# Optimization experiments

Measured on AMD Instinct MI355X. Metric: run time of the kernel, lower is better.

## Reference

```python
import jax, jax.numpy as jnp
import numpy as np

NH, NKV, HD = 16, 4, 64   # n_heads, n_kv_heads, head_dim
N_REP = NH // NKV
EPS = 1e-6


def rms_norm(x, w):
    var = jnp.mean(x.astype(jnp.float32) ** 2, axis=-1, keepdims=True)
    return (x.astype(jnp.float32) * jax.lax.rsqrt(var + EPS)).astype(x.dtype) * w


def rotate_half(x):
    x1, x2 = jnp.split(x, 2, axis=-1)
    return jnp.concatenate([-x2, x1], axis=-1)


def setup_inputs() -> dict:
    key = jax.random.key(0)
    ks = jax.random.split(key, 6)
    B, S, H = 2, 2048, 2048
    x = jax.random.normal(ks[0], (B, S, H), dtype=jnp.float32)
    # RoPE tables [S, HD]
    inv_freq = 1.0 / (10000.0 ** (jnp.arange(0, HD, 2, dtype=jnp.float32) / HD))
    freqs = jnp.arange(S, dtype=jnp.float32)[:, None] * inv_freq[None, :]
    emb = jnp.concatenate([freqs, freqs], axis=-1)
    cos, sin = jnp.cos(emb), jnp.sin(emb)
    scale = 0.02
    wq = jax.random.normal(ks[1], (H, NH * HD), dtype=jnp.float32) * scale
    wk = jax.random.normal(ks[2], (H, NKV * HD), dtype=jnp.float32) * scale
    wv = jax.random.normal(ks[3], (H, NKV * HD), dtype=jnp.float32) * scale
    wo = jax.random.normal(ks[4], (NH * HD, H), dtype=jnp.float32) * scale
    q_norm_w = jnp.ones((HD,), dtype=jnp.float32)
    k_norm_w = jnp.ones((HD,), dtype=jnp.float32)
    return {"x": x, "cos": cos, "sin": sin, "wq": wq, "wk": wk, "wv": wv,
            "wo": wo, "q_norm_w": q_norm_w, "k_norm_w": k_norm_w}


def reference(x, cos, sin, wq, wk, wv, wo, q_norm_w, k_norm_w):
    B, S, H = x.shape
    # QKV projections + per-head RMSNorm on q/k
    q = rms_norm((x @ wq).reshape(B, S, NH, HD), q_norm_w)
    k = rms_norm((x @ wk).reshape(B, S, NKV, HD), k_norm_w)
    v = (x @ wv).reshape(B, S, NKV, HD)
    # RoPE (broadcast over heads)
    c = cos[None, :S, None, :]
    s = sin[None, :S, None, :]
    q = q * c + rotate_half(q) * s
    k = k * c + rotate_half(k) * s
    # prefill with S == window_size: no KV eviction, T == S -> causal mask
    k = jnp.repeat(k, N_REP, axis=2)  # [B,S,NH,HD]
    v = jnp.repeat(v, N_REP, axis=2)
    scores = jnp.einsum('bqhd,bkhd->bhqk', q, k) / jnp.sqrt(jnp.float32(HD))
    causal = jnp.triu(jnp.full((S, S), -jnp.inf, dtype=scores.dtype), 1)
    scores = scores + causal
    attn = jax.nn.softmax(scores.astype(jnp.float32), axis=-1).astype(q.dtype)
    out = jnp.einsum('bhqk,bkhd->bqhd', attn, v).reshape(B, S, NH * HD)
    return out @ wo
```

## Files before the change

kernel.cpp:

```cpp
#include <hip/hip_runtime.h>

typedef float floatx4 __attribute__((ext_vector_type(4)));
typedef __bf16 bfx8 __attribute__((ext_vector_type(8)));
typedef __bf16 bfx4 __attribute__((ext_vector_type(4)));

constexpr int B_ = 2, S_ = 2048, H_ = 2048, NH_ = 16, NKV_ = 4, HD_ = 64;
constexpr int M_ = B_ * S_;
constexpr int NQKV_ = NH_ * HD_ + 2 * NKV_ * HD_;
constexpr int HQ_ = NH_ * HD_;
constexpr int XP_ = 2112;
constexpr int AP_ = 1088;
constexpr int VP_ = 2112;
constexpr int QKV_ELEMS_ = M_ * NQKV_;

#define GLB(p) ((const __attribute__((address_space(1))) void*)(p))
#define LDS(p) ((__attribute__((address_space(3))) void*)(p))

__global__ __launch_bounds__(256) void prep_kernel(const float* __restrict__ x,
                                                   const float* __restrict__ wq,
                                                   const float* __restrict__ wk,
                                                   const float* __restrict__ wv,
                                                   const float* __restrict__ wo,
                                                   __bf16* __restrict__ xbf,
                                                   __bf16* __restrict__ wqkvT,
                                                   __bf16* __restrict__ woT) {
  __shared__ float tile[32][33];
  int bid = blockIdx.x;
  if (bid < M_) {
    const float4* s = (const float4*)(x + (size_t)bid * H_);
    __bf16* d = xbf + (size_t)bid * XP_;
#pragma unroll
    for (int i = 0; i < 2; i++) {
      int c = i * 256 + threadIdx.x;
      float4 v = s[c];
      bfx4 o;
      o[0] = (__bf16)v.x; o[1] = (__bf16)v.y; o[2] = (__bf16)v.z; o[3] = (__bf16)v.w;
      *(bfx4*)(d + c * 4) = o;
    }
    return;
  }
  bid -= M_;
  const float* src; __bf16* dst; int N, dstOff, pitch, nbx;
  if (bid < 2048)      { src = wq; dst = wqkvT; N = 1024; dstOff = 0;    pitch = XP_; nbx = 32; }
  else if (bid < 2560) { bid -= 2048; src = wk; dst = wqkvT; N = 256; dstOff = 1024; pitch = XP_; nbx = 8; }
  else if (bid < 3072) { bid -= 2560; src = wv; dst = wqkvT; N = 256; dstOff = 1280; pitch = XP_; nbx = 8; }
  else                 { bid -= 3072; src = wo; dst = woT;   N = 2048; dstOff = 0;   pitch = AP_; nbx = 64; }
  int n0 = (bid % nbx) * 32, k0 = (bid / nbx) * 32;
  int tx = threadIdx.x & 31, ty = threadIdx.x >> 5;
#pragma unroll
  for (int r = 0; r < 32; r += 8)
    tile[ty + r][tx] = src[(size_t)(k0 + ty + r) * N + n0 + tx];
  __syncthreads();
#pragma unroll
  for (int r = 0; r < 32; r += 8)
    dst[(size_t)(n0 + ty + r + dstOff) * pitch + k0 + tx] = (__bf16)tile[tx][ty + r];
}

__global__ __launch_bounds__(512) void gemm_bf16_f32(const __bf16* __restrict__ A,
                                                     const __bf16* __restrict__ Bt,
                                                     float* __restrict__ C,
                                                     int M, int N, int K,
                                                     int lda, int ldb, int ldc,
                                                     unsigned long long cstride) {
  __shared__ __align__(16) __bf16 As[256 * 64];
  __shared__ __align__(16) __bf16 Bs[128 * 64];
  int wid = threadIdx.x >> 6, lane = threadIdx.x & 63;
  int l15 = lane & 15, quad = lane >> 4;
  int wm = (wid >> 1) * 64, wn = (wid & 1) * 64;
  int m0 = blockIdx.y * 256, n0 = blockIdx.x * 128;
  int kb0 = blockIdx.z * K;
  C += (size_t)blockIdx.z * cstride;
  int srow_off = lane >> 3;
  int gphys = lane & 7;
  floatx4 acc[4][4] = {};
  for (int kb = kb0; kb < kb0 + K; kb += 64) {
#pragma unroll
    for (int j = 0; j < 4; j++) {
      int rbase = j * 64 + wid * 8;
      int row = rbase + srow_off;
      int glog = gphys ^ (row & 7);
      const __bf16* ga = &A[(size_t)(m0 + row) * lda + kb + glog * 8];
      __builtin_amdgcn_global_load_lds(GLB(ga), LDS(&As[rbase * 64]), 16, 0, 0);
    }
#pragma unroll
    for (int j = 0; j < 2; j++) {
      int rbase = j * 64 + wid * 8;
      int row = rbase + srow_off;
      int glog = gphys ^ (row & 7);
      const __bf16* gb = &Bt[(size_t)(n0 + row) * ldb + kb + glog * 8];
      __builtin_amdgcn_global_load_lds(GLB(gb), LDS(&Bs[rbase * 64]), 16, 0, 0);
    }
    __syncthreads();
#pragma unroll
    for (int kk = 0; kk < 64; kk += 32) {
      int cgq = (kk >> 3) + quad;
      bfx8 af[4], bfr[4];
#pragma unroll
      for (int mi = 0; mi < 4; mi++) {
        int row = wm + mi * 16 + l15;
        af[mi] = *(const bfx8*)&As[row * 64 + (cgq ^ (row & 7)) * 8];
      }
#pragma unroll
      for (int ni = 0; ni < 4; ni++) {
        int row = wn + ni * 16 + l15;
        bfr[ni] = *(const bfx8*)&Bs[row * 64 + (cgq ^ (row & 7)) * 8];
      }
#pragma unroll
      for (int mi = 0; mi < 4; mi++)
#pragma unroll
        for (int ni = 0; ni < 4; ni++)
          acc[mi][ni] = __builtin_amdgcn_mfma_f32_16x16x32_bf16(af[mi], bfr[ni], acc[mi][ni], 0, 0, 0);
    }
    __syncthreads();
  }
#pragma unroll
  for (int mi = 0; mi < 4; mi++)
#pragma unroll
    for (int ni = 0; ni < 4; ni++) {
      int row = m0 + wm + mi * 16 + quad * 4;
      int coln = n0 + wn + ni * 16 + l15;
#pragma unroll
      for (int r = 0; r < 4; r++)
        C[(size_t)(row + r) * ldc + coln] = acc[mi][ni][r];
    }
}

__global__ __launch_bounds__(256) void norm_rope_kernel(const float* __restrict__ qkv,
                                                        const float* __restrict__ cosT,
                                                        const float* __restrict__ sinT,
                                                        const float* __restrict__ qw,
                                                        const float* __restrict__ kw,
                                                        __bf16* __restrict__ Qo,
                                                        __bf16* __restrict__ Ko,
                                                        __bf16* __restrict__ VTo) {
  int s = blockIdx.x, b = blockIdx.y;
  int wid = threadIdx.x >> 6, lane = threadIdx.x & 63;
  const float* rowp = qkv + (size_t)(b * S_ + s) * NQKV_;
  const float* rowp2 = rowp + QKV_ELEMS_;
  float c = cosT[s * HD_ + lane];
  float sn = sinT[s * HD_ + lane];
#pragma unroll
  for (int it = 0; it < 5; it++) {
    int hh = it * 4 + wid;
    int idx = hh * 64 + lane;
    float v = rowp[idx] + rowp2[idx];
    float ss = v * v;
#pragma unroll
    for (int off = 1; off < 64; off <<= 1) ss += __shfl_xor(ss, off);
    float rs = rsqrtf(ss * (1.0f / 64.0f) + 1e-6f);
    const float* w = (hh < 16) ? qw : kw;
    float nv = v * rs * w[lane];
    float other = __shfl_xor(nv, 32);
    float rot = (lane < 32) ? -other : other;
    float outv = nv * c + rot * sn;
    if (hh < 16)
      Qo[(((size_t)b * NH_ + hh) * S_ + s) * HD_ + lane] = (__bf16)outv;
    else
      Ko[(((size_t)b * NKV_ + (hh - 16)) * S_ + s) * HD_ + lane] = (__bf16)outv;
  }
  {
    int idx = (20 + wid) * 64 + lane;
    float v = rowp[idx] + rowp2[idx];
    VTo[(((size_t)b * NKV_ + wid) * HD_ + lane) * VP_ + s] = (__bf16)v;
  }
}

__global__ __launch_bounds__(256, 4) void attn_kernel(const __bf16* __restrict__ Q,
                                                      const __bf16* __restrict__ Kc,
                                                      const __bf16* __restrict__ VT,
                                                      __bf16* __restrict__ Ob) {
  int px = blockIdx.x, h = blockIdx.y, b = blockIdx.z;
  int u = (px + 2 * (h & 7)) & 31;
  int qt = (((h >> 3) ^ b) & 1) ? (31 - u) : u;
  int wid = threadIdx.x >> 6, lane = threadIdx.x & 63;
  int l15 = lane & 15, quad = lane >> 4;
  int q0 = qt * 64 + wid * 16;
  int kvh = h >> 2;
  const __bf16* Qh = Q + (((size_t)b * NH_ + h) * S_ + q0) * HD_;
  const __bf16* Kh = Kc + ((size_t)b * NKV_ + kvh) * S_ * HD_;
  const __bf16* Vh = VT + ((size_t)b * NKV_ + kvh) * (size_t)HD_ * VP_;
  __shared__ __align__(16) __bf16 Ks[64][72];
  __shared__ __align__(16) __bf16 Vs[64][72];
  __shared__ __align__(16) __bf16 Pst[4][16][72];
  __bf16 (*P)[72] = Pst[wid];

  int srow = threadIdx.x >> 3;
  int scol = (threadIdx.x & 7) * 8;

  bfx8 qf0, qf1;
  {
    const __bf16* qp = Qh + l15 * HD_ + quad * 8;
    qf0 = *(const bfx8*)qp;
    qf1 = *(const bfx8*)(qp + 32);
  }
  floatx4 oacc[4] = {};
  float ps = 0.f;
  int ntiles = qt + 1;
  bfx8 kpre0, kpre1, vpre0, vpre1;
  kpre0 = *(const bfx8*)&Kh[(size_t)srow * HD_ + scol];
  kpre1 = *(const bfx8*)&Kh[(size_t)(srow + 32) * HD_ + scol];
  vpre0 = *(const bfx8*)&Vh[(size_t)srow * VP_ + scol];
  vpre1 = *(const bfx8*)&Vh[(size_t)(srow + 32) * VP_ + scol];
  for (int kt = 0; kt < ntiles; kt++) {
    int kv0 = kt * 64;
    int dq = q0 - kv0;
    __syncthreads();
    *(bfx8*)&Ks[srow][scol] = kpre0;
    *(bfx8*)&Ks[srow + 32][scol] = kpre1;
    *(bfx8*)&Vs[srow][scol] = vpre0;
    *(bfx8*)&Vs[srow + 32][scol] = vpre1;
    __syncthreads();
    if (kt + 1 < ntiles) {
      int kn = kv0 + 64;
      kpre0 = *(const bfx8*)&Kh[(size_t)(kn + srow) * HD_ + scol];
      kpre1 = *(const bfx8*)&Kh[(size_t)(kn + srow + 32) * HD_ + scol];
      vpre0 = *(const bfx8*)&Vh[(size_t)srow * VP_ + kn + scol];
      vpre1 = *(const bfx8*)&Vh[(size_t)(srow + 32) * VP_ + kn + scol];
    }
    floatx4 sf[4];
#pragma unroll
    for (int nt = 0; nt < 4; nt++) {
      bfx8 kf0 = *(const bfx8*)&Ks[nt * 16 + l15][quad * 8];
      bfx8 kf1 = *(const bfx8*)&Ks[nt * 16 + l15][32 + quad * 8];
      floatx4 z = {0.f, 0.f, 0.f, 0.f};
      z = __builtin_amdgcn_mfma_f32_16x16x32_bf16(kf0, qf0, z, 0, 0, 0);
      sf[nt] = __builtin_amdgcn_mfma_f32_16x16x32_bf16(kf1, qf1, z, 0, 0, 0);
    }
#pragma unroll
    for (int nt = 0; nt < 4; nt++) {
      bfx4 pk;
#pragma unroll
      for (int r = 0; r < 4; r++) {
        int kvrel = nt * 16 + quad * 4 + r;
        float p = __expf(sf[nt][r] * 0.125f);
        p = (kvrel - l15 > dq) ? 0.f : p;
        ps += p;
        pk[r] = (__bf16)p;
      }
      *(bfx4*)&P[l15][nt * 16 + quad * 4] = pk;
    }
    bfx8 pa0 = *(const bfx8*)&P[l15][quad * 8];
    bfx8 pa1 = *(const bfx8*)&P[l15][32 + quad * 8];
#pragma unroll
    for (int ot = 0; ot < 4; ot++) {
      bfx8 vf0 = *(const bfx8*)&Vs[ot * 16 + l15][quad * 8];
      bfx8 vf1 = *(const bfx8*)&Vs[ot * 16 + l15][32 + quad * 8];
      oacc[ot] = __builtin_amdgcn_mfma_f32_16x16x32_bf16(pa0, vf0, oacc[ot], 0, 0, 0);
      oacc[ot] = __builtin_amdgcn_mfma_f32_16x16x32_bf16(pa1, vf1, oacc[ot], 0, 0, 0);
    }
  }
  ps += __shfl_xor(ps, 16);
  ps += __shfl_xor(ps, 32);
  float rl[4];
#pragma unroll
  for (int r = 0; r < 4; r++) rl[r] = 1.0f / __shfl(ps, quad * 4 + r);
#pragma unroll
  for (int ot = 0; ot < 4; ot++)
#pragma unroll
    for (int r = 0; r < 4; r++) {
      float val = oacc[ot][r] * rl[r];
      Ob[((size_t)b * S_ + q0 + quad * 4 + r) * AP_ + h * HD_ + ot * 16 + l15] = (__bf16)val;
    }
}

extern "C" void kernel_launch(void* const* d_in, const int* in_sizes, int n_in,
                              void* d_out, int out_size, void* d_ws, size_t ws_size,
                              hipStream_t stream) {
  const float* x   = (const float*)d_in[0];
  const float* cosT = (const float*)d_in[1];
  const float* sinT = (const float*)d_in[2];
  const float* wq  = (const float*)d_in[3];
  const float* wk  = (const float*)d_in[4];
  const float* wv  = (const float*)d_in[5];
  const float* wo  = (const float*)d_in[6];
  const float* qw  = (const float*)d_in[7];
  const float* kw  = (const float*)d_in[8];
  float* out = (float*)d_out;

  char* w = (char*)d_ws;
  __bf16* xbf   = (__bf16*)(w);
  __bf16* Qb    = (__bf16*)(w);
  __bf16* Kb    = (__bf16*)(w + 8388608);
  __bf16* VTb   = (__bf16*)(w + 10485760);
  __bf16* wqkvT = (__bf16*)(w + 17301504);
  __bf16* woT   = (__bf16*)(w + 23789568);
  float*  qkv   = (float*) (w + 28246016);
  __bf16* attnO = (__bf16*)(w + 28246016);

  prep_kernel<<<M_ + 5120, 256, 0, stream>>>(x, wq, wk, wv, wo, xbf, wqkvT, woT);
  gemm_bf16_f32<<<dim3(NQKV_ / 128, M_ / 256, 2), 512, 0, stream>>>(
      xbf, wqkvT, qkv, M_, NQKV_, H_ / 2, XP_, XP_, NQKV_, (unsigned long long)QKV_ELEMS_);
  norm_rope_kernel<<<dim3(S_, B_), 256, 0, stream>>>(qkv, cosT, sinT, qw, kw, Qb, Kb, VTb);
  attn_kernel<<<dim3(32, NH_, B_), 256, 0, stream>>>(Qb, Kb, VTb, attnO);
  gemm_bf16_f32<<<dim3(H_ / 128, M_ / 256, 1), 512, 0, stream>>>(
      attnO, woT, out, M_, H_, HQ_, AP_, AP_, H_, 0ull);
}
```

Baseline: 224.3 us.

## Fuse RMSNorm and RoPE epilogue into QKV GEMM, drop split-K

```diff
diff --git a/kernel.cpp b/kernel.cpp
--- a/kernel.cpp
+++ b/kernel.cpp
@@ -11,7 +11,6 @@
 constexpr int XP_ = 2112;
 constexpr int AP_ = 1088;
 constexpr int VP_ = 2112;
-constexpr int QKV_ELEMS_ = M_ * NQKV_;
 
 #define GLB(p) ((const __attribute__((address_space(1))) void*)(p))
 #define LDS(p) ((__attribute__((address_space(3))) void*)(p))
@@ -56,24 +55,126 @@
     dst[(size_t)(n0 + ty + r + dstOff) * pitch + k0 + tx] = (__bf16)tile[tx][ty + r];
 }
 
+__global__ __launch_bounds__(256) void gemm_qkv_fused(const __bf16* __restrict__ A,
+                                                      const __bf16* __restrict__ Bt,
+                                                      const float* __restrict__ cosT,
+                                                      const float* __restrict__ sinT,
+                                                      const float* __restrict__ qw,
+                                                      const float* __restrict__ kw,
+                                                      __bf16* __restrict__ Qo,
+                                                      __bf16* __restrict__ Ko,
+                                                      __bf16* __restrict__ VTo) {
+  __shared__ __align__(16) __bf16 As[128 * 64];
+  __shared__ __align__(16) __bf16 Bs[128 * 64];
+  int wid = threadIdx.x >> 6, lane = threadIdx.x & 63;
+  int l15 = lane & 15, quad = lane >> 4;
+  int wm = (wid >> 1) * 64, wn = (wid & 1) * 64;
+  int m0 = blockIdx.y * 128, n0 = blockIdx.x * 128;
+  int srow_off = lane >> 3;
+  int gphys = lane & 7;
+  floatx4 acc[4][4] = {};
+  for (int kb = 0; kb < H_; kb += 64) {
+#pragma unroll
+    for (int j = 0; j < 4; j++) {
+      int rbase = wid * 32 + j * 8;
+      int row = rbase + srow_off;
+      int glog = gphys ^ (row & 7);
+      const __bf16* ga = &A[(size_t)(m0 + row) * XP_ + kb + glog * 8];
+      const __bf16* gb = &Bt[(size_t)(n0 + row) * XP_ + kb + glog * 8];
+      __builtin_amdgcn_global_load_lds(GLB(ga), LDS(&As[rbase * 64]), 16, 0, 0);
+      __builtin_amdgcn_global_load_lds(GLB(gb), LDS(&Bs[rbase * 64]), 16, 0, 0);
+    }
+    __syncthreads();
+#pragma unroll
+    for (int kk = 0; kk < 64; kk += 32) {
+      int cgq = (kk >> 3) + quad;
+      bfx8 af[4], bfr[4];
+#pragma unroll
+      for (int mi = 0; mi < 4; mi++) {
+        int row = wm + mi * 16 + l15;
+        af[mi] = *(const bfx8*)&As[row * 64 + (cgq ^ (row & 7)) * 8];
+      }
+#pragma unroll
+      for (int ni = 0; ni < 4; ni++) {
+        int row = wn + ni * 16 + l15;
+        bfr[ni] = *(const bfx8*)&Bs[row * 64 + (cgq ^ (row & 7)) * 8];
+      }
+#pragma unroll
+      for (int mi = 0; mi < 4; mi++)
+#pragma unroll
+        for (int ni = 0; ni < 4; ni++)
+          acc[mi][ni] = __builtin_amdgcn_mfma_f32_16x16x32_bf16(af[mi], bfr[ni], acc[mi][ni], 0, 0, 0);
+    }
+    __syncthreads();
+  }
+  int hh = (n0 + wn) >> 6;
+  int b = m0 >> 11;
+  if (hh < 20) {
+    const float* wptr = (hh < 16) ? qw : kw;
+    float wv4[4];
+#pragma unroll
+    for (int ni = 0; ni < 4; ni++) wv4[ni] = wptr[ni * 16 + l15];
+    __bf16* outp = (hh < 16) ? (Qo + (((size_t)b * NH_ + hh) * S_) * HD_)
+                             : (Ko + (((size_t)b * NKV_ + (hh - 16)) * S_) * HD_);
+#pragma unroll
+    for (int mi = 0; mi < 4; mi++) {
+#pragma unroll
+      for (int r = 0; r < 4; r++) {
+        float ssum = acc[mi][0][r] * acc[mi][0][r] + acc[mi][1][r] * acc[mi][1][r] +
+                     acc[mi][2][r] * acc[mi][2][r] + acc[mi][3][r] * acc[mi][3][r];
+        ssum += __shfl_xor(ssum, 1);
+        ssum += __shfl_xor(ssum, 2);
+        ssum += __shfl_xor(ssum, 4);
+        ssum += __shfl_xor(ssum, 8);
+        float rs = rsqrtf(ssum * (1.0f / 64.0f) + 1e-6f);
+        int row = wm + mi * 16 + quad * 4 + r;
+        int s = (m0 & 2047) + row;
+        float nv[4];
+#pragma unroll
+        for (int ni = 0; ni < 4; ni++) nv[ni] = acc[mi][ni][r] * rs * wv4[ni];
+#pragma unroll
+        for (int ni = 0; ni < 4; ni++) {
+          int d = ni * 16 + l15;
+          float c = cosT[s * HD_ + d];
+          float sn = sinT[s * HD_ + d];
+          float partner = nv[ni ^ 2];
+          float rot = (ni < 2) ? -partner : partner;
+          outp[(size_t)s * HD_ + d] = (__bf16)(nv[ni] * c + rot * sn);
+        }
+      }
+    }
+  } else {
+    __bf16* vtp = VTo + ((size_t)b * NKV_ + (hh - 20)) * (size_t)HD_ * VP_;
+#pragma unroll
+    for (int mi = 0; mi < 4; mi++)
+#pragma unroll
+      for (int r = 0; r < 4; r++) {
+        int row = wm + mi * 16 + quad * 4 + r;
+        int s = (m0 & 2047) + row;
+#pragma unroll
+        for (int ni = 0; ni < 4; ni++) {
+          int d = ni * 16 + l15;
+          vtp[(size_t)d * VP_ + s] = (__bf16)acc[mi][ni][r];
+        }
+      }
+  }
+}
+
 __global__ __launch_bounds__(512) void gemm_bf16_f32(const __bf16* __restrict__ A,
                                                      const __bf16* __restrict__ Bt,
                                                      float* __restrict__ C,
                                                      int M, int N, int K,
-                                                     int lda, int ldb, int ldc,
-                                                     unsigned long long cstride) {
+                                                     int lda, int ldb, int ldc) {
   __shared__ __align__(16) __bf16 As[256 * 64];
   __shared__ __align__(16) __bf16 Bs[128 * 64];
   int wid = threadIdx.x >> 6, lane = threadIdx.x & 63;
   int l15 = lane & 15, quad = lane >> 4;
   int wm = (wid >> 1) * 64, wn = (wid & 1) * 64;
   int m0 = blockIdx.y * 256, n0 = blockIdx.x * 128;
-  int kb0 = blockIdx.z * K;
-  C += (size_t)blockIdx.z * cstride;
   int srow_off = lane >> 3;
   int gphys = lane & 7;
   floatx4 acc[4][4] = {};
-  for (int kb = kb0; kb < kb0 + K; kb += 64) {
+  for (int kb = 0; kb < K; kb += 64) {
 #pragma unroll
     for (int j = 0; j < 4; j++) {
       int rbase = j * 64 + wid * 8;
@@ -123,46 +224,6 @@
       for (int r = 0; r < 4; r++)
         C[(size_t)(row + r) * ldc + coln] = acc[mi][ni][r];
     }
-}
-
-__global__ __launch_bounds__(256) void norm_rope_kernel(const float* __restrict__ qkv,
-                                                        const float* __restrict__ cosT,
-                                                        const float* __restrict__ sinT,
-                                                        const float* __restrict__ qw,
-                                                        const float* __restrict__ kw,
-                                                        __bf16* __restrict__ Qo,
-                                                        __bf16* __restrict__ Ko,
-                                                        __bf16* __restrict__ VTo) {
-  int s = blockIdx.x, b = blockIdx.y;
-  int wid = threadIdx.x >> 6, lane = threadIdx.x & 63;
-  const float* rowp = qkv + (size_t)(b * S_ + s) * NQKV_;
-  const float* rowp2 = rowp + QKV_ELEMS_;
-  float c = cosT[s * HD_ + lane];
-  float sn = sinT[s * HD_ + lane];
-#pragma unroll
-  for (int it = 0; it < 5; it++) {
-    int hh = it * 4 + wid;
-    int idx = hh * 64 + lane;
-    float v = rowp[idx] + rowp2[idx];
-    float ss = v * v;
-#pragma unroll
-    for (int off = 1; off < 64; off <<= 1) ss += __shfl_xor(ss, off);
-    float rs = rsqrtf(ss * (1.0f / 64.0f) + 1e-6f);
-    const float* w = (hh < 16) ? qw : kw;
-    float nv = v * rs * w[lane];
-    float other = __shfl_xor(nv, 32);
-    float rot = (lane < 32) ? -other : other;
-    float outv = nv * c + rot * sn;
-    if (hh < 16)
-      Qo[(((size_t)b * NH_ + hh) * S_ + s) * HD_ + lane] = (__bf16)outv;
-    else
-      Ko[(((size_t)b * NKV_ + (hh - 16)) * S_ + s) * HD_ + lane] = (__bf16)outv;
-  }
-  {
-    int idx = (20 + wid) * 64 + lane;
-    float v = rowp[idx] + rowp2[idx];
-    VTo[(((size_t)b * NKV_ + wid) * HD_ + lane) * VP_ + s] = (__bf16)v;
-  }
 }
 
 __global__ __launch_bounds__(256, 4) void attn_kernel(const __bf16* __restrict__ Q,
@@ -279,19 +340,17 @@
 
   char* w = (char*)d_ws;
   __bf16* xbf   = (__bf16*)(w);
-  __bf16* Qb    = (__bf16*)(w);
-  __bf16* Kb    = (__bf16*)(w + 8388608);
-  __bf16* VTb   = (__bf16*)(w + 10485760);
   __bf16* wqkvT = (__bf16*)(w + 17301504);
   __bf16* woT   = (__bf16*)(w + 23789568);
-  float*  qkv   = (float*) (w + 28246016);
-  __bf16* attnO = (__bf16*)(w + 28246016);
+  __bf16* Qb    = (__bf16*)(w + 28246016);
+  __bf16* Kb    = (__bf16*)(w + 36634624);
+  __bf16* VTb   = (__bf16*)(w + 38731776);
+  __bf16* attnO = (__bf16*)(w + 40894464);
 
   prep_kernel<<<M_ + 5120, 256, 0, stream>>>(x, wq, wk, wv, wo, xbf, wqkvT, woT);
-  gemm_bf16_f32<<<dim3(NQKV_ / 128, M_ / 256, 2), 512, 0, stream>>>(
-      xbf, wqkvT, qkv, M_, NQKV_, H_ / 2, XP_, XP_, NQKV_, (unsigned long long)QKV_ELEMS_);
-  norm_rope_kernel<<<dim3(S_, B_), 256, 0, stream>>>(qkv, cosT, sinT, qw, kw, Qb, Kb, VTb);
+  gemm_qkv_fused<<<dim3(NQKV_ / 128, M_ / 128), 256, 0, stream>>>(
+      xbf, wqkvT, cosT, sinT, qw, kw, Qb, Kb, VTb);
   attn_kernel<<<dim3(32, NH_, B_), 256, 0, stream>>>(Qb, Kb, VTb, attnO);
-  gemm_bf16_f32<<<dim3(H_ / 128, M_ / 256, 1), 512, 0, stream>>>(
-      attnO, woT, out, M_, H_, HQ_, AP_, AP_, H_, 0ull);
-}
+  gemm_bf16_f32<<<dim3(H_ / 128, M_ / 256), 512, 0, stream>>>(
+      attnO, woT, out, M_, H_, HQ_, AP_, AP_, H_);
+}
```

Result: faster. 218.7 us (-2.5%).
